# Optimization experiments

Hardware: AMD Instinct MI355X
Metric: run time of the kernel (lower is better)

## Reference

```python
import jax, jax.numpy as jnp
import numpy as np

EMBED = 768
HEADS = 12
D_K = EMBED // HEADS  # 64


def setup_inputs() -> dict:
    key = jax.random.key(0)
    ks = jax.random.split(key, 9)
    w_scale = EMBED ** -0.5
    inp = {
        "x": jax.random.normal(ks[0], (128, 256, 1, EMBED), dtype=jnp.float32),
        "Wq": jax.random.normal(ks[1], (EMBED, EMBED), dtype=jnp.float32) * w_scale,
        "bq": jax.random.normal(ks[2], (EMBED,), dtype=jnp.float32) * 0.02,
        "Wk": jax.random.normal(ks[3], (EMBED, EMBED), dtype=jnp.float32) * w_scale,
        "bk": jax.random.normal(ks[4], (EMBED,), dtype=jnp.float32) * 0.02,
        "Wv": jax.random.normal(ks[5], (EMBED, EMBED), dtype=jnp.float32) * w_scale,
        "bv": jax.random.normal(ks[6], (EMBED,), dtype=jnp.float32) * 0.02,
        "Wo": jax.random.normal(ks[7], (EMBED, EMBED), dtype=jnp.float32) * w_scale,
        "bo": jax.random.normal(ks[8], (EMBED,), dtype=jnp.float32) * 0.02,
    }
    return inp


def reference(x, Wq, bq, Wk, bk, Wv, bv, Wo, bo):
    # x: (n_rows r, n_cols i/j, batch n, embed)
    R, C, B, E = x.shape
    H, Dk = HEADS, D_K
    # tied-row scaling: d_k^{-1/2} / sqrt(n_rows)
    scaling = (Dk ** -0.5) / np.sqrt(R).astype(np.float32)

    q = (x @ Wq.T + bq).reshape(R, C, B, H, Dk) * scaling
    k = (x @ Wk.T + bk).reshape(R, C, B, H, Dk)
    v = (x @ Wv.T + bv).reshape(R, C, B, H, Dk)

    # scores summed over rows r and head dim d -> (h, n, i, j)
    scores = jnp.einsum('rinhd,rjnhd->hnij', q, k)
    probs = jax.nn.softmax(scores, axis=-1)  # dropout p=0 -> identity

    # shared attention applied per row
    c = jnp.einsum('hnij,rjnhd->rinhd', probs, v).reshape(R, C, B, E)
    out = c @ Wo.T + bo
    return (out, probs)
```

## Files before the change

### kernel.cpp

```cpp
#include <hip/hip_runtime.h>
#include <math.h>

typedef short bf16x8 __attribute__((ext_vector_type(8)));
typedef float f32x4 __attribute__((ext_vector_type(4)));
typedef unsigned short ushort8 __attribute__((ext_vector_type(8)));

constexpr int R = 128, Cc = 256, E = 768, H = 12;
constexpr int M = R * Cc;
constexpr size_t TOK = (size_t)M * E;

__device__ __forceinline__ unsigned short f2b(float f) {
  unsigned int u = __float_as_uint(f);
  u += 0x7fff + ((u >> 16) & 1);
  return (unsigned short)(u >> 16);
}

__device__ __forceinline__ void ldst16(const unsigned short* g, unsigned short* l) {
  __builtin_amdgcn_global_load_lds(
      (const __attribute__((address_space(1))) unsigned int*)g,
      (__attribute__((address_space(3))) unsigned int*)l, 16, 0, 0);
}

__global__ __launch_bounds__(256) void cvt_bf16(const float* __restrict__ in,
                                                unsigned short* __restrict__ out,
                                                int n8) {
  int i = blockIdx.x * 256 + threadIdx.x;
  if (i >= n8) return;
  const float4* p = (const float4*)in;
  float4 a = p[2 * i], b = p[2 * i + 1];
  ushort8 o;
  o[0] = f2b(a.x); o[1] = f2b(a.y); o[2] = f2b(a.z); o[3] = f2b(a.w);
  o[4] = f2b(b.x); o[5] = f2b(b.y); o[6] = f2b(b.z); o[7] = f2b(b.w);
  ((ushort8*)out)[i] = o;
}

template <int MODE>
__global__ __launch_bounds__(256) void proj_mfma(
    const unsigned short* __restrict__ A, const unsigned short* __restrict__ B,
    const float* __restrict__ bias, void* __restrict__ Yv, float scale) {
  constexpr int K = 768, N = 768;
  __shared__ unsigned short As[128 * 32];
  __shared__ unsigned short Bs[128 * 32];
  const int tid = threadIdx.x, wv = tid >> 6, ln = tid & 63;
  const int n0 = blockIdx.x * 128, m0 = blockIdx.y * 128;
  const int wm = (wv & 1) * 64, wn = (wv >> 1) * 64;
  const int srow = ln >> 2, scol = (ln & 3) * 8;
  f32x4 acc[4][4] = {};
  for (int k0 = 0; k0 < K; k0 += 32) {
    __syncthreads();
#pragma unroll
    for (int t = 0; t < 2; ++t) {
      const int ch = wv * 2 + t;
      const int row = ch * 16 + srow;
      ldst16(A + (size_t)(m0 + row) * K + k0 + scol, As + ch * 512 + ln * 8);
      ldst16(B + (size_t)(n0 + row) * K + k0 + scol, Bs + ch * 512 + ln * 8);
    }
    __syncthreads();
    bf16x8 a[4], b[4];
#pragma unroll
    for (int i = 0; i < 4; ++i)
      a[i] = *(const bf16x8*)(As + (wm + i * 16 + (ln & 15)) * 32 + (ln >> 4) * 8);
#pragma unroll
    for (int j = 0; j < 4; ++j)
      b[j] = *(const bf16x8*)(Bs + (wn + j * 16 + (ln & 15)) * 32 + (ln >> 4) * 8);
#pragma unroll
    for (int i = 0; i < 4; ++i)
#pragma unroll
      for (int j = 0; j < 4; ++j)
        acc[i][j] = __builtin_amdgcn_mfma_f32_16x16x32_bf16(a[i], b[j], acc[i][j], 0, 0, 0);
  }
#pragma unroll
  for (int j = 0; j < 4; ++j) {
    const int n = n0 + wn + j * 16 + (ln & 15);
    const float bn = bias[n];
#pragma unroll
    for (int i = 0; i < 4; ++i) {
#pragma unroll
      for (int r = 0; r < 4; ++r) {
        const int m = m0 + wm + i * 16 + (ln >> 4) * 4 + r;
        const float v = (acc[i][j][r] + bn) * scale;
        if (MODE == 0)      ((unsigned short*)Yv)[(size_t)m * N + n] = f2b(v);
        else if (MODE == 1) ((unsigned short*)Yv)[(size_t)n * M + m] = f2b(v);
        else                ((float*)Yv)[(size_t)m * N + n] = v;
      }
    }
  }
}

__global__ __launch_bounds__(256) void qk_mfma(const unsigned short* __restrict__ q,
                                               const unsigned short* __restrict__ k,
                                               float* __restrict__ Sp) {
  __shared__ unsigned short As[64 * 64];
  __shared__ unsigned short Bs[64 * 64];
  const int tid = threadIdx.x, wv = tid >> 6, ln = tid & 63;
  const int i0 = (blockIdx.x & 3) * 64, j0 = (blockIdx.x >> 2) * 64;
  const int h = blockIdx.y, kc = blockIdx.z;
  const int wm = (wv & 1) * 32, wn = (wv >> 1) * 32;
  const int srow = ln >> 3, scol = (ln & 7) * 8;
  f32x4 acc[2][2] = {};
  for (int rr = 0; rr < 32; ++rr) {
    const int r = kc * 32 + rr;
    __syncthreads();
#pragma unroll
    for (int t = 0; t < 2; ++t) {
      const int ch = wv * 2 + t;
      const int row = ch * 8 + srow;
      ldst16(q + (size_t)(r * Cc + i0 + row) * E + h * 64 + scol, As + ch * 512 + ln * 8);
      ldst16(k + (size_t)(r * Cc + j0 + row) * E + h * 64 + scol, Bs + ch * 512 + ln * 8);
    }
    __syncthreads();
#pragma unroll
    for (int dk = 0; dk < 2; ++dk) {
      bf16x8 a[2], b[2];
#pragma unroll
      for (int i = 0; i < 2; ++i)
        a[i] = *(const bf16x8*)(As + (wm + i * 16 + (ln & 15)) * 64 + dk * 32 + (ln >> 4) * 8);
#pragma unroll
      for (int j = 0; j < 2; ++j)
        b[j] = *(const bf16x8*)(Bs + (wn + j * 16 + (ln & 15)) * 64 + dk * 32 + (ln >> 4) * 8);
#pragma unroll
      for (int i = 0; i < 2; ++i)
#pragma unroll
        for (int j = 0; j < 2; ++j)
          acc[i][j] = __builtin_amdgcn_mfma_f32_16x16x32_bf16(a[i], b[j], acc[i][j], 0, 0, 0);
    }
  }
  const size_t base = ((size_t)kc * H + h) * Cc * Cc;
#pragma unroll
  for (int i = 0; i < 2; ++i)
#pragma unroll
    for (int j = 0; j < 2; ++j)
#pragma unroll
      for (int r4 = 0; r4 < 4; ++r4) {
        const int ii = i0 + wm + i * 16 + (ln >> 4) * 4 + r4;
        const int jj = j0 + wn + j * 16 + (ln & 15);
        Sp[base + (size_t)ii * Cc + jj] = acc[i][j][r4];
      }
}

__global__ __launch_bounds__(256) void softmax_k(const float* __restrict__ Sp,
                                                 float* __restrict__ P,
                                                 unsigned short* __restrict__ Pb) {
  const int row = blockIdx.x, j = threadIdx.x;
  const size_t stride = (size_t)H * Cc * Cc;
  const size_t base = (size_t)row * Cc + j;
  float s = Sp[base] + Sp[base + stride] + Sp[base + 2 * stride] + Sp[base + 3 * stride];
  float m = s;
#pragma unroll
  for (int o = 32; o > 0; o >>= 1) m = fmaxf(m, __shfl_xor(m, o));
  __shared__ float sm[4], ss[4];
  const int wid = j >> 6, lane = j & 63;
  if (lane == 0) sm[wid] = m;
  __syncthreads();
  m = fmaxf(fmaxf(sm[0], sm[1]), fmaxf(sm[2], sm[3]));
  float e = expf(s - m);
  float t = e;
#pragma unroll
  for (int o = 32; o > 0; o >>= 1) t += __shfl_xor(t, o);
  if (lane == 0) ss[wid] = t;
  __syncthreads();
  t = ss[0] + ss[1] + ss[2] + ss[3];
  const float p = e / t;
  P[base] = p;
  Pb[base] = f2b(p);
}

__global__ __launch_bounds__(256) void pv_mfma(const unsigned short* __restrict__ P,
                                               const unsigned short* __restrict__ V,
                                               unsigned short* __restrict__ Co) {
  __shared__ unsigned short As[64 * 64];
  __shared__ unsigned short Bs[64 * 64];
  const int tid = threadIdx.x, wv = tid >> 6, ln = tid & 63;
  const int i0 = blockIdx.x * 64;
  const int r = blockIdx.y, h = blockIdx.z;
  const int wm = (wv & 1) * 32, wn = (wv >> 1) * 32;
  const int srow = ln >> 3, scol = (ln & 7) * 8;
  f32x4 acc[2][2] = {};
  for (int jc = 0; jc < 4; ++jc) {
    const int j0 = jc * 64;
    __syncthreads();
#pragma unroll
    for (int t = 0; t < 2; ++t) {
      const int ch = wv * 2 + t;
      const int row = ch * 8 + srow;
      ldst16(P + ((size_t)h * Cc + i0 + row) * Cc + j0 + scol, As + ch * 512 + ln * 8);
      ldst16(V + (size_t)(h * 64 + row) * M + r * Cc + j0 + scol, Bs + ch * 512 + ln * 8);
    }
    __syncthreads();
#pragma unroll
    for (int dk = 0; dk < 2; ++dk) {
      bf16x8 a[2], b[2];
#pragma unroll
      for (int i = 0; i < 2; ++i)
        a[i] = *(const bf16x8*)(As + (wm + i * 16 + (ln & 15)) * 64 + dk * 32 + (ln >> 4) * 8);
#pragma unroll
      for (int j = 0; j < 2; ++j)
        b[j] = *(const bf16x8*)(Bs + (wn + j * 16 + (ln & 15)) * 64 + dk * 32 + (ln >> 4) * 8);
#pragma unroll
      for (int i = 0; i < 2; ++i)
#pragma unroll
        for (int j = 0; j < 2; ++j)
          acc[i][j] = __builtin_amdgcn_mfma_f32_16x16x32_bf16(a[i], b[j], acc[i][j], 0, 0, 0);
    }
  }
#pragma unroll
  for (int i = 0; i < 2; ++i)
#pragma unroll
    for (int j = 0; j < 2; ++j)
#pragma unroll
      for (int r4 = 0; r4 < 4; ++r4) {
        const int mm = i0 + wm + i * 16 + (ln >> 4) * 4 + r4;
        const int nn = wn + j * 16 + (ln & 15);
        Co[((size_t)r * Cc + mm) * E + h * 64 + nn] = f2b(acc[i][j][r4]);
      }
}

extern "C" void kernel_launch(void* const* d_in, const int* in_sizes, int n_in,
                              void* d_out, int out_size, void* d_ws, size_t ws_size,
                              hipStream_t stream) {
  const float* x  = (const float*)d_in[0];
  const float* Wq = (const float*)d_in[1];
  const float* bq = (const float*)d_in[2];
  const float* Wk = (const float*)d_in[3];
  const float* bk = (const float*)d_in[4];
  const float* Wv = (const float*)d_in[5];
  const float* bv = (const float*)d_in[6];
  const float* Wo = (const float*)d_in[7];
  const float* bo = (const float*)d_in[8];
  float* out = (float*)d_out;
  float* probs = out + TOK;

  char* ws = (char*)d_ws;
  unsigned short* x_bf  = (unsigned short*)(ws);
  unsigned short* q_bf  = (unsigned short*)(ws + 50331648);
  unsigned short* k_bf  = (unsigned short*)(ws + 100663296);
  unsigned short* vT_bf = (unsigned short*)(ws + 150994944);
  unsigned short* Wq_bf = (unsigned short*)(ws + 201326592);
  unsigned short* Wk_bf = Wq_bf + 589824;
  unsigned short* Wv_bf = Wk_bf + 589824;
  unsigned short* Wo_bf = Wv_bf + 589824;
  float* S_part         = (float*)(ws + 206045184);
  unsigned short* P_bf  = (unsigned short*)(ws + 218628096);
  unsigned short* c_bf  = q_bf;

  const float scaling = 0.125f / sqrtf(128.f);

  cvt_bf16<<<12288, 256, 0, stream>>>(x, x_bf, 3145728);
  cvt_bf16<<<288, 256, 0, stream>>>(Wq, Wq_bf, 73728);
  cvt_bf16<<<288, 256, 0, stream>>>(Wk, Wk_bf, 73728);
  cvt_bf16<<<288, 256, 0, stream>>>(Wv, Wv_bf, 73728);
  cvt_bf16<<<288, 256, 0, stream>>>(Wo, Wo_bf, 73728);

  dim3 gp(6, 256);
  proj_mfma<0><<<gp, 256, 0, stream>>>(x_bf, Wq_bf, bq, q_bf, scaling);
  proj_mfma<0><<<gp, 256, 0, stream>>>(x_bf, Wk_bf, bk, k_bf, 1.0f);
  proj_mfma<1><<<gp, 256, 0, stream>>>(x_bf, Wv_bf, bv, vT_bf, 1.0f);

  qk_mfma<<<dim3(16, H, 4), 256, 0, stream>>>(q_bf, k_bf, S_part);
  softmax_k<<<H * Cc, 256, 0, stream>>>(S_part, probs, P_bf);
  pv_mfma<<<dim3(4, R, H), 256, 0, stream>>>(P_bf, vT_bf, c_bf);

  proj_mfma<2><<<gp, 256, 0, stream>>>(c_bf, Wo_bf, bo, out, 1.0f);
}
```

Baseline: 540.8 us.

## Fuse QKV projection and relayout Q/K/V per head for large-tile attention GEMMs

Fuses the three input projections into one launch that writes Q and K in a head-major [h][col][row*64+d] layout and V as [h][row*64+d][col]. With that layout QK^T becomes a long-K GEMM over rows and head dims, split 8 ways, and PV becomes a plain 128x128-tile GEMM with K=256. Both can reuse the shared 128x128 MFMA tile routine. Adds grouped block swizzling for L2 locality and reuses workspace regions for the score partials. The trade-offs are scattered 2-byte stores in the projection epilogue and twice as many split-K partials for softmax to sum.

```diff
diff --git a/kernel.cpp b/kernel.cpp
--- a/kernel.cpp
+++ b/kernel.cpp
@@ -4,6 +4,7 @@
 typedef short bf16x8 __attribute__((ext_vector_type(8)));
 typedef float f32x4 __attribute__((ext_vector_type(4)));
 typedef unsigned short ushort8 __attribute__((ext_vector_type(8)));
+typedef unsigned short ushort4v __attribute__((ext_vector_type(4)));
 
 constexpr int R = 128, Cc = 256, E = 768, H = 12;
 constexpr int M = R * Cc;
@@ -34,26 +35,20 @@
   ((ushort8*)out)[i] = o;
 }
 
-template <int MODE>
-__global__ __launch_bounds__(256) void proj_mfma(
-    const unsigned short* __restrict__ A, const unsigned short* __restrict__ B,
-    const float* __restrict__ bias, void* __restrict__ Yv, float scale) {
-  constexpr int K = 768, N = 768;
-  __shared__ unsigned short As[128 * 32];
-  __shared__ unsigned short Bs[128 * 32];
-  const int tid = threadIdx.x, wv = tid >> 6, ln = tid & 63;
-  const int n0 = blockIdx.x * 128, m0 = blockIdx.y * 128;
-  const int wm = (wv & 1) * 64, wn = (wv >> 1) * 64;
+__device__ __forceinline__ void gemm128(const unsigned short* __restrict__ A, int lda,
+                                        const unsigned short* __restrict__ B, int ldb,
+                                        int K, unsigned short* As, unsigned short* Bs,
+                                        int wv, int ln, int wm, int wn,
+                                        f32x4 (&acc)[4][4]) {
   const int srow = ln >> 2, scol = (ln & 3) * 8;
-  f32x4 acc[4][4] = {};
   for (int k0 = 0; k0 < K; k0 += 32) {
     __syncthreads();
 #pragma unroll
     for (int t = 0; t < 2; ++t) {
       const int ch = wv * 2 + t;
       const int row = ch * 16 + srow;
-      ldst16(A + (size_t)(m0 + row) * K + k0 + scol, As + ch * 512 + ln * 8);
-      ldst16(B + (size_t)(n0 + row) * K + k0 + scol, Bs + ch * 512 + ln * 8);
+      ldst16(A + (size_t)row * lda + k0 + scol, As + ch * 512 + ln * 8);
+      ldst16(B + (size_t)row * ldb + k0 + scol, Bs + ch * 512 + ln * 8);
     }
     __syncthreads();
     bf16x8 a[4], b[4];
@@ -69,73 +64,82 @@
       for (int j = 0; j < 4; ++j)
         acc[i][j] = __builtin_amdgcn_mfma_f32_16x16x32_bf16(a[i], b[j], acc[i][j], 0, 0, 0);
   }
-#pragma unroll
-  for (int j = 0; j < 4; ++j) {
-    const int n = n0 + wn + j * 16 + (ln & 15);
-    const float bn = bias[n];
+}
+
+__global__ __launch_bounds__(256) void qkv_proj(
+    const unsigned short* __restrict__ A, const unsigned short* __restrict__ B,
+    const float* __restrict__ bq, const float* __restrict__ bk,
+    const float* __restrict__ bv, unsigned short* __restrict__ q2,
+    unsigned short* __restrict__ k2, unsigned short* __restrict__ v3, float scaling) {
+  __shared__ unsigned short As[128 * 32];
+  __shared__ unsigned short Bs[128 * 32];
+  const int tid = threadIdx.x, wv = tid >> 6, ln = tid & 63;
+  const unsigned p = blockIdx.x + blockIdx.y * 18;
+  const unsigned l = (p & 7) * 576 + (p >> 3);
+  const int bx = l % 18, by = l / 18;
+  const int n0 = bx * 128, m0 = by * 128;
+  const int wm = (wv & 1) * 64, wn = (wv >> 1) * 64;
+  f32x4 acc[4][4] = {};
+  gemm128(A + (size_t)m0 * 768, 768, B + (size_t)n0 * 768, 768, 768,
+          As, Bs, wv, ln, wm, wn, acc);
+
+  const int region = bx / 6;
+  const float* bias = region == 0 ? bq : (region == 1 ? bk : bv);
+  const float sc = region == 0 ? scaling : 1.0f;
+  const int nq0 = n0 - region * 768;
+#pragma unroll
+  for (int j = 0; j < 4; ++j) {
+    const int np = nq0 + wn + j * 16 + (ln & 15);
+    const int h = np >> 6, d = np & 63;
+    const float bn = bias[np];
 #pragma unroll
     for (int i = 0; i < 4; ++i) {
+      const int mb = m0 + wm + i * 16 + (ln >> 4) * 4;
+      if (region < 2) {
+        unsigned short* dst = region == 0 ? q2 : k2;
+#pragma unroll
+        for (int r = 0; r < 4; ++r) {
+          const int m = mb + r;
+          const int ic = m & 255, rr = m >> 8;
+          dst[(size_t)h * 2097152 + (size_t)ic * 8192 + rr * 64 + d] =
+              f2b((acc[i][j][r] + bn) * sc);
+        }
+      } else {
+        const int jc = mb & 255, rr = mb >> 8;
+        ushort4v o;
+#pragma unroll
+        for (int r = 0; r < 4; ++r) o[r] = f2b(acc[i][j][r] + bn);
+        *(ushort4v*)(v3 + (size_t)h * 2097152 + ((size_t)rr * 64 + d) * 256 + jc) = o;
+      }
+    }
+  }
+}
+
+__global__ __launch_bounds__(256) void qk_gemm(const unsigned short* __restrict__ q2,
+                                               const unsigned short* __restrict__ k2,
+                                               float* __restrict__ Sp) {
+  __shared__ unsigned short As[128 * 32];
+  __shared__ unsigned short Bs[128 * 32];
+  const int tid = threadIdx.x, wv = tid >> 6, ln = tid & 63;
+  const int i0 = (blockIdx.x & 1) * 128, j0 = (blockIdx.x >> 1) * 128;
+  const int h = blockIdx.y, kc = blockIdx.z;
+  const int wm = (wv & 1) * 64, wn = (wv >> 1) * 64;
+  f32x4 acc[4][4] = {};
+  const unsigned short* Ap = q2 + (size_t)h * 2097152 + (size_t)i0 * 8192 + kc * 1024;
+  const unsigned short* Bp = k2 + (size_t)h * 2097152 + (size_t)j0 * 8192 + kc * 1024;
+  gemm128(Ap, 8192, Bp, 8192, 1024, As, Bs, wv, ln, wm, wn, acc);
+  float* out = Sp + ((size_t)kc * H + h) * 65536;
+#pragma unroll
+  for (int j = 0; j < 4; ++j) {
+    const int jj = j0 + wn + j * 16 + (ln & 15);
+#pragma unroll
+    for (int i = 0; i < 4; ++i)
 #pragma unroll
       for (int r = 0; r < 4; ++r) {
-        const int m = m0 + wm + i * 16 + (ln >> 4) * 4 + r;
-        const float v = (acc[i][j][r] + bn) * scale;
-        if (MODE == 0)      ((unsigned short*)Yv)[(size_t)m * N + n] = f2b(v);
-        else if (MODE == 1) ((unsigned short*)Yv)[(size_t)n * M + m] = f2b(v);
-        else                ((float*)Yv)[(size_t)m * N + n] = v;
-      }
-    }
-  }
-}
-
-__global__ __launch_bounds__(256) void qk_mfma(const unsigned short* __restrict__ q,
-                                               const unsigned short* __restrict__ k,
-                                               float* __restrict__ Sp) {
-  __shared__ unsigned short As[64 * 64];
-  __shared__ unsigned short Bs[64 * 64];
-  const int tid = threadIdx.x, wv = tid >> 6, ln = tid & 63;
-  const int i0 = (blockIdx.x & 3) * 64, j0 = (blockIdx.x >> 2) * 64;
-  const int h = blockIdx.y, kc = blockIdx.z;
-  const int wm = (wv & 1) * 32, wn = (wv >> 1) * 32;
-  const int srow = ln >> 3, scol = (ln & 7) * 8;
-  f32x4 acc[2][2] = {};
-  for (int rr = 0; rr < 32; ++rr) {
-    const int r = kc * 32 + rr;
-    __syncthreads();
-#pragma unroll
-    for (int t = 0; t < 2; ++t) {
-      const int ch = wv * 2 + t;
-      const int row = ch * 8 + srow;
-      ldst16(q + (size_t)(r * Cc + i0 + row) * E + h * 64 + scol, As + ch * 512 + ln * 8);
-      ldst16(k + (size_t)(r * Cc + j0 + row) * E + h * 64 + scol, Bs + ch * 512 + ln * 8);
-    }
-    __syncthreads();
-#pragma unroll
-    for (int dk = 0; dk < 2; ++dk) {
-      bf16x8 a[2], b[2];
-#pragma unroll
-      for (int i = 0; i < 2; ++i)
-        a[i] = *(const bf16x8*)(As + (wm + i * 16 + (ln & 15)) * 64 + dk * 32 + (ln >> 4) * 8);
-#pragma unroll
-      for (int j = 0; j < 2; ++j)
-        b[j] = *(const bf16x8*)(Bs + (wn + j * 16 + (ln & 15)) * 64 + dk * 32 + (ln >> 4) * 8);
-#pragma unroll
-      for (int i = 0; i < 2; ++i)
-#pragma unroll
-        for (int j = 0; j < 2; ++j)
-          acc[i][j] = __builtin_amdgcn_mfma_f32_16x16x32_bf16(a[i], b[j], acc[i][j], 0, 0, 0);
-    }
-  }
-  const size_t base = ((size_t)kc * H + h) * Cc * Cc;
-#pragma unroll
-  for (int i = 0; i < 2; ++i)
-#pragma unroll
-    for (int j = 0; j < 2; ++j)
-#pragma unroll
-      for (int r4 = 0; r4 < 4; ++r4) {
-        const int ii = i0 + wm + i * 16 + (ln >> 4) * 4 + r4;
-        const int jj = j0 + wn + j * 16 + (ln & 15);
-        Sp[base + (size_t)ii * Cc + jj] = acc[i][j][r4];
-      }
+        const int ii = i0 + wm + i * 16 + (ln >> 4) * 4 + r;
+        out[(size_t)ii * 256 + jj] = acc[i][j][r];
+      }
+  }
 }
 
 __global__ __launch_bounds__(256) void softmax_k(const float* __restrict__ Sp,
@@ -144,7 +148,9 @@
   const int row = blockIdx.x, j = threadIdx.x;
   const size_t stride = (size_t)H * Cc * Cc;
   const size_t base = (size_t)row * Cc + j;
-  float s = Sp[base] + Sp[base + stride] + Sp[base + 2 * stride] + Sp[base + 3 * stride];
+  float s = 0.f;
+#pragma unroll
+  for (int c = 0; c < 8; ++c) s += Sp[base + c * stride];
   float m = s;
 #pragma unroll
   for (int o = 32; o > 0; o >>= 1) m = fmaxf(m, __shfl_xor(m, o));
@@ -165,54 +171,62 @@
   Pb[base] = f2b(p);
 }
 
-__global__ __launch_bounds__(256) void pv_mfma(const unsigned short* __restrict__ P,
+__global__ __launch_bounds__(256) void pv_gemm(const unsigned short* __restrict__ P,
                                                const unsigned short* __restrict__ V,
                                                unsigned short* __restrict__ Co) {
-  __shared__ unsigned short As[64 * 64];
-  __shared__ unsigned short Bs[64 * 64];
-  const int tid = threadIdx.x, wv = tid >> 6, ln = tid & 63;
-  const int i0 = blockIdx.x * 64;
-  const int r = blockIdx.y, h = blockIdx.z;
-  const int wm = (wv & 1) * 32, wn = (wv >> 1) * 32;
-  const int srow = ln >> 3, scol = (ln & 7) * 8;
-  f32x4 acc[2][2] = {};
-  for (int jc = 0; jc < 4; ++jc) {
-    const int j0 = jc * 64;
-    __syncthreads();
-#pragma unroll
-    for (int t = 0; t < 2; ++t) {
-      const int ch = wv * 2 + t;
-      const int row = ch * 8 + srow;
-      ldst16(P + ((size_t)h * Cc + i0 + row) * Cc + j0 + scol, As + ch * 512 + ln * 8);
-      ldst16(V + (size_t)(h * 64 + row) * M + r * Cc + j0 + scol, Bs + ch * 512 + ln * 8);
-    }
-    __syncthreads();
-#pragma unroll
-    for (int dk = 0; dk < 2; ++dk) {
-      bf16x8 a[2], b[2];
-#pragma unroll
-      for (int i = 0; i < 2; ++i)
-        a[i] = *(const bf16x8*)(As + (wm + i * 16 + (ln & 15)) * 64 + dk * 32 + (ln >> 4) * 8);
-#pragma unroll
-      for (int j = 0; j < 2; ++j)
-        b[j] = *(const bf16x8*)(Bs + (wn + j * 16 + (ln & 15)) * 64 + dk * 32 + (ln >> 4) * 8);
-#pragma unroll
-      for (int i = 0; i < 2; ++i)
-#pragma unroll
-        for (int j = 0; j < 2; ++j)
-          acc[i][j] = __builtin_amdgcn_mfma_f32_16x16x32_bf16(a[i], b[j], acc[i][j], 0, 0, 0);
-    }
-  }
-#pragma unroll
-  for (int i = 0; i < 2; ++i)
-#pragma unroll
-    for (int j = 0; j < 2; ++j)
-#pragma unroll
-      for (int r4 = 0; r4 < 4; ++r4) {
-        const int mm = i0 + wm + i * 16 + (ln >> 4) * 4 + r4;
-        const int nn = wn + j * 16 + (ln & 15);
-        Co[((size_t)r * Cc + mm) * E + h * 64 + nn] = f2b(acc[i][j][r4]);
-      }
+  __shared__ unsigned short As[128 * 32];
+  __shared__ unsigned short Bs[128 * 32];
+  const int tid = threadIdx.x, wv = tid >> 6, ln = tid & 63;
+  const unsigned p = blockIdx.x + blockIdx.y * 128;
+  const unsigned l = (p & 7) * 192 + (p >> 3);
+  const int bx = l & 127, h = l >> 7;
+  const int i0 = (bx & 1) * 128, n0 = (bx >> 1) * 128;
+  const int wm = (wv & 1) * 64, wn = (wv >> 1) * 64;
+  f32x4 acc[4][4] = {};
+  const unsigned short* Ap = P + (size_t)h * 65536 + (size_t)i0 * 256;
+  const unsigned short* Bp = V + (size_t)h * 2097152 + (size_t)n0 * 256;
+  gemm128(Ap, 256, Bp, 256, 256, As, Bs, wv, ln, wm, wn, acc);
+#pragma unroll
+  for (int j = 0; j < 4; ++j) {
+    const int n = n0 + wn + j * 16 + (ln & 15);
+    const int rr = n >> 6, d = n & 63;
+#pragma unroll
+    for (int i = 0; i < 4; ++i)
+#pragma unroll
+      for (int r = 0; r < 4; ++r) {
+        const int ii = i0 + wm + i * 16 + (ln >> 4) * 4 + r;
+        Co[((size_t)rr * 256 + ii) * 768 + h * 64 + d] = f2b(acc[i][j][r]);
+      }
+  }
+}
+
+__global__ __launch_bounds__(256) void o_proj(const unsigned short* __restrict__ A,
+                                              const unsigned short* __restrict__ B,
+                                              const float* __restrict__ bias,
+                                              float* __restrict__ Y) {
+  __shared__ unsigned short As[128 * 32];
+  __shared__ unsigned short Bs[128 * 32];
+  const int tid = threadIdx.x, wv = tid >> 6, ln = tid & 63;
+  const unsigned p = blockIdx.x + blockIdx.y * 6;
+  const unsigned l = (p & 7) * 192 + (p >> 3);
+  const int bx = l % 6, by = l / 6;
+  const int n0 = bx * 128, m0 = by * 128;
+  const int wm = (wv & 1) * 64, wn = (wv >> 1) * 64;
+  f32x4 acc[4][4] = {};
+  gemm128(A + (size_t)m0 * 768, 768, B + (size_t)n0 * 768, 768, 768,
+          As, Bs, wv, ln, wm, wn, acc);
+#pragma unroll
+  for (int j = 0; j < 4; ++j) {
+    const int n = n0 + wn + j * 16 + (ln & 15);
+    const float bn = bias[n];
+#pragma unroll
+    for (int i = 0; i < 4; ++i)
+#pragma unroll
+      for (int r = 0; r < 4; ++r) {
+        const int m = m0 + wm + i * 16 + (ln >> 4) * 4 + r;
+        Y[(size_t)m * 768 + n] = acc[i][j][r] + bn;
+      }
+  }
 }
 
 extern "C" void kernel_launch(void* const* d_in, const int* in_sizes, int n_in,
@@ -232,16 +246,16 @@
 
   char* ws = (char*)d_ws;
   unsigned short* x_bf  = (unsigned short*)(ws);
-  unsigned short* q_bf  = (unsigned short*)(ws + 50331648);
-  unsigned short* k_bf  = (unsigned short*)(ws + 100663296);
-  unsigned short* vT_bf = (unsigned short*)(ws + 150994944);
+  unsigned short* q2    = (unsigned short*)(ws + 50331648);
+  unsigned short* k2    = (unsigned short*)(ws + 100663296);
+  unsigned short* v3    = (unsigned short*)(ws + 150994944);
   unsigned short* Wq_bf = (unsigned short*)(ws + 201326592);
   unsigned short* Wk_bf = Wq_bf + 589824;
   unsigned short* Wv_bf = Wk_bf + 589824;
   unsigned short* Wo_bf = Wv_bf + 589824;
-  float* S_part         = (float*)(ws + 206045184);
-  unsigned short* P_bf  = (unsigned short*)(ws + 218628096);
-  unsigned short* c_bf  = q_bf;
+  float* S_part         = (float*)(ws);
+  unsigned short* P_bf  = (unsigned short*)(ws + 25165824);
+  unsigned short* c_bf  = q2;
 
   const float scaling = 0.125f / sqrtf(128.f);
 
@@ -251,14 +265,12 @@
   cvt_bf16<<<288, 256, 0, stream>>>(Wv, Wv_bf, 73728);
   cvt_bf16<<<288, 256, 0, stream>>>(Wo, Wo_bf, 73728);
 
-  dim3 gp(6, 256);
-  proj_mfma<0><<<gp, 256, 0, stream>>>(x_bf, Wq_bf, bq, q_bf, scaling);
-  proj_mfma<0><<<gp, 256, 0, stream>>>(x_bf, Wk_bf, bk, k_bf, 1.0f);
-  proj_mfma<1><<<gp, 256, 0, stream>>>(x_bf, Wv_bf, bv, vT_bf, 1.0f);
-
-  qk_mfma<<<dim3(16, H, 4), 256, 0, stream>>>(q_bf, k_bf, S_part);
+  qkv_proj<<<dim3(18, 256), 256, 0, stream>>>(x_bf, Wq_bf, bq, bk, bv,
+                                              q2, k2, v3, scaling);
+
+  qk_gemm<<<dim3(4, H, 8), 256, 0, stream>>>(q2, k2, S_part);
   softmax_k<<<H * Cc, 256, 0, stream>>>(S_part, probs, P_bf);
-  pv_mfma<<<dim3(4, R, H), 256, 0, stream>>>(P_bf, vT_bf, c_bf);
-
-  proj_mfma<2><<<gp, 256, 0, stream>>>(c_bf, Wo_bf, bo, out, 1.0f);
-}
+  pv_gemm<<<dim3(128, H), 256, 0, stream>>>(P_bf, v3, c_bf);
+
+  o_proj<<<dim3(6, 256), 256, 0, stream>>>(c_bf, Wo_bf, bo, out);
+}
```

Result: no change. 545.9 us (+0.9%).
